# Optimization experiments

Measured on AMD Instinct MI355X. Metric: run time of the kernel, lower is better.

## Reference

```python
import jax, jax.numpy as jnp
import numpy as np

S, B, D, Z, C, H = 256, 1024, 64, 32, 64, 128
L = 2 * S + 3  # len(ext_ts); _xs[0::2][1:-1] must match xs -> L = 2*S+3


def setup_inputs() -> dict:
    key = jax.random.key(0)
    ks = jax.random.split(key, 16)

    def xavier(k, out_d, in_d):
        lim = float(np.sqrt(6.0 / (in_d + out_d)))
        return jax.random.uniform(k, (out_d, in_d), minval=-lim, maxval=lim, dtype=jnp.float32)

    bias = lambda n: jnp.full((n,), 0.01, jnp.float32)  # m.bias.data.fill_(0.01)

    return {
        "xs": jax.random.normal(ks[0], (S, B, D), jnp.float32),
        "ext_ts": jnp.arange(L, dtype=jnp.float32) * 0.01,  # spacing <= dt=0.02 -> 1 euler step/interval
        "eps_z0": jax.random.normal(ks[1], (B, Z), jnp.float32),
        "dW": jax.random.normal(ks[2], (L - 1, B, Z), jnp.float32),  # standard normal; scaled by sqrt(dt) inside
        "gru_Wih": xavier(ks[3], 3 * H, D),
        "gru_Whh": xavier(ks[4], 3 * H, H),
        "gru_bih": jnp.zeros((3 * H,), jnp.float32),
        "gru_bhh": jnp.zeros((3 * H,), jnp.float32),
        "enc_W": xavier(ks[5], C, H), "enc_b": bias(C),
        "qz0_W": xavier(ks[6], 2 * Z, C), "qz0_b": bias(2 * Z),
        "f_W1": xavier(ks[7], H, Z + 1), "f_b1": bias(H),
        "f_W2": xavier(ks[8], H, H), "f_b2": bias(H),
        "f_W3": xavier(ks[9], Z, H), "f_b3": bias(Z),
        "g_W1": xavier(ks[10], H, Z + 1), "g_b1": bias(H),
        "g_W2": xavier(ks[11], Z, H), "g_b2": bias(Z),
        "proj_W": xavier(ks[12], D, Z), "proj_b": bias(D),
        "pz0_mean": jnp.zeros((1, Z), jnp.float32),
        "pz0_logstd": jnp.zeros((1, Z), jnp.float32),
    }


def reference(xs, ext_ts, eps_z0, dW, gru_Wih, gru_Whh, gru_bih, gru_bhh,
              enc_W, enc_b, qz0_W, qz0_b,
              f_W1, f_b1, f_W2, f_b2, f_W3, f_b3,
              g_W1, g_b1, g_W2, g_b2,
              proj_W, proj_b, pz0_mean, pz0_logstd):
    nb = xs.shape[1]
    # ---- Encoder: GRU over time-reversed xs; only ctx[0] (after flip-back) is
    # used, which equals lin(final hidden of the reversed-sequence GRU).
    x_rev = xs[::-1]
    gi_all = jnp.einsum('sbd,hd->sbh', x_rev, gru_Wih) + gru_bih  # (S,B,3H)

    def gru_step(h, gi_t):
        gh = h @ gru_Whh.T + gru_bhh
        i_r, i_z, i_n = jnp.split(gi_t, 3, axis=-1)
        h_r, h_z, h_n = jnp.split(gh, 3, axis=-1)
        r = jax.nn.sigmoid(i_r + h_r)
        zg = jax.nn.sigmoid(i_z + h_z)
        n = jnp.tanh(i_n + r * h_n)
        return (1.0 - zg) * n + zg * h, None

    hT, _ = jax.lax.scan(gru_step, jnp.zeros((nb, gru_Whh.shape[1]), xs.dtype), gi_all)
    ctx0 = hT @ enc_W.T + enc_b

    # ---- q(z0) and reparameterized sample
    q = ctx0 @ qz0_W.T + qz0_b
    qz0_mean, qz0_logstd = jnp.split(q, 2, axis=1)
    z0 = qz0_mean + jnp.exp(qz0_logstd) * eps_z0

    # ---- Euler-Maruyama SDE integration (diagonal noise), one step per interval
    dts = ext_ts[1:] - ext_ts[:-1]

    def sde_step(z, inp):
        t, dt, dw = inp
        tcol = jnp.broadcast_to(t.reshape(1, 1), (z.shape[0], 1)).astype(z.dtype)
        tz = jnp.concatenate([tcol, z], axis=1)  # (B, Z+1)
        h1 = jax.nn.relu(tz @ f_W1.T + f_b1)
        h2 = jax.nn.relu(h1 @ f_W2.T + f_b2)
        drift = h2 @ f_W3.T + f_b3
        gh = jax.nn.relu(tz @ g_W1.T + g_b1)
        diff = gh @ g_W2.T + g_b2
        z_new = z + drift * dt + diff * (jnp.sqrt(dt) * dw)
        return z_new, z_new

    _, zs_rest = jax.lax.scan(sde_step, z0, (ext_ts[:-1], dts, dW))
    zs = jnp.concatenate([z0[None], zs_rest], axis=0)  # (L,B,Z)

    # ---- project to data space and compute losses
    xs_hat = jnp.einsum('lbz,dz->lbd', zs, proj_W) + proj_b
    recon_xs = xs_hat[0::2][1:-1]   # (S,B,D)
    interp_xs = xs_hat[1::2][1:-1]  # (S-1,B,D)
    recon_loss = jnp.mean((recon_xs - xs) ** 2)

    # KL( N(qm, e^qls) || N(pm, e^pls) ), summed over latent, averaged over batch
    kl = (pz0_logstd - qz0_logstd
          + (jnp.exp(2.0 * qz0_logstd) + (qz0_mean - pz0_mean) ** 2)
          / (2.0 * jnp.exp(2.0 * pz0_logstd)) - 0.5)
    logqp0 = jnp.mean(jnp.sum(kl, axis=1))
    return recon_loss, logqp0, interp_xs
```

## Files before the change

### kernel.cpp

```cpp
#include <hip/hip_runtime.h>

typedef _Float16 f16;
typedef _Float16 h2 __attribute__((ext_vector_type(2)));
typedef _Float16 h8 __attribute__((ext_vector_type(8)));
typedef _Float16 v8h __attribute__((ext_vector_type(8)));
typedef _Float16 v4h __attribute__((ext_vector_type(4)));
typedef float    f4 __attribute__((ext_vector_type(4)));
typedef float    v4f __attribute__((ext_vector_type(4)));
typedef float    f2 __attribute__((ext_vector_type(2)));

#define S_  256
#define B_  1024
#define D_  64
#define H_  128
#define Z_  32
#define BD_ (B_*D_)
#define NSTEP 514

#define BAR() do { \
  asm volatile("s_waitcnt lgkmcnt(0)" ::: "memory"); \
  __builtin_amdgcn_s_barrier(); \
} while (0)

__device__ __forceinline__ h8 ld8(const float* p) {
  f4 a = *(const f4*)p;
  f4 b = *(const f4*)(p + 4);
  h8 w;
  w[0]=(f16)a[0]; w[1]=(f16)a[1]; w[2]=(f16)a[2]; w[3]=(f16)a[3];
  w[4]=(f16)b[0]; w[5]=(f16)b[1]; w[6]=(f16)b[2]; w[7]=(f16)b[3];
  return w;
}

__device__ __forceinline__ float sigm(float x) { return 1.f / (1.f + __expf(-x)); }
__device__ __forceinline__ float tanh_(float x) {
  float e = __expf(-2.f * fabsf(x));
  float t = (1.f - e) / (1.f + e);
  return copysignf(t, x);
}

__global__ __launch_bounds__(256, 1) void gru_mfma_kernel(
    const float* __restrict__ xs, const float* __restrict__ Wih,
    const float* __restrict__ Whh, const float* __restrict__ bih,
    const float* __restrict__ bhh, float* __restrict__ hT)
{
  __shared__ f16 hB[2][16][136];

  const int t    = threadIdx.x;
  const int wid  = t >> 6;
  const int lane = t & 63;
  const int lr = lane & 15;
  const int lg = lane >> 4;
  const int r0 = blockIdx.x * 16;

  v8h whhR[2][4], whhZ[2][4], whhN[2][4];
  v8h wihR[2][2], wihZ[2][2], wihN[2][2];
  #pragma unroll
  for (int tt = 0; tt < 2; ++tt) {
    const int nr = wid*32 + tt*16 + lr;
    #pragma unroll
    for (int ks = 0; ks < 4; ++ks) {
      whhR[tt][ks] = ld8(Whh + (      nr)*H_ + ks*32 + lg*8);
      whhZ[tt][ks] = ld8(Whh + (128 + nr)*H_ + ks*32 + lg*8);
      whhN[tt][ks] = ld8(Whh + (256 + nr)*H_ + ks*32 + lg*8);
    }
    #pragma unroll
    for (int ks = 0; ks < 2; ++ks) {
      wihR[tt][ks] = ld8(Wih + (      nr)*D_ + ks*32 + lg*8);
      wihZ[tt][ks] = ld8(Wih + (128 + nr)*D_ + ks*32 + lg*8);
      wihN[tt][ks] = ld8(Wih + (256 + nr)*D_ + ks*32 + lg*8);
    }
  }
  v4f birh[2], bizh[2], binv[2], bhnv[2];
  #pragma unroll
  for (int tt = 0; tt < 2; ++tt) {
    const int nb = wid*32 + tt*16 + lg*4;
    v4f a = *(const v4f*)&bih[nb],     b = *(const v4f*)&bhh[nb];
    v4f c = *(const v4f*)&bih[128+nb], d = *(const v4f*)&bhh[128+nb];
    birh[tt] = a + b;
    bizh[tt] = c + d;
    binv[tt] = *(const v4f*)&bih[256+nb];
    bhnv[tt] = *(const v4f*)&bhh[256+nb];
  }

  for (int i = t; i < 16*136; i += 256) ((f16*)hB[0])[i] = (f16)0.f;
  v4f hm[2] = { {0.f,0.f,0.f,0.f}, {0.f,0.f,0.f,0.f} };
  const v4f zero4 = {0.f, 0.f, 0.f, 0.f};

  v8h bx0 = ld8(xs + (S_-1)*BD_ + (r0+lr)*D_ + lg*8);
  v8h bx1 = ld8(xs + (S_-1)*BD_ + (r0+lr)*D_ + 32 + lg*8);
  __syncthreads();

  int p = 0;
  #pragma unroll 1
  for (int s = 0; s < S_; ++s) {
    v8h nx0 = bx0, nx1 = bx1;
    if (s < S_-1) {
      const float* xp = xs + (S_-2-s)*BD_ + (r0+lr)*D_;
      nx0 = ld8(xp + lg*8);
      nx1 = ld8(xp + 32 + lg*8);
    }
    v8h bh[4];
    #pragma unroll
    for (int ks = 0; ks < 4; ++ks)
      bh[ks] = *(const v8h*)&hB[p][lr][ks*32 + lg*8];

    #pragma unroll
    for (int tt = 0; tt < 2; ++tt) {
      v4f ar  = __builtin_amdgcn_mfma_f32_16x16x32_f16(wihR[tt][0], bx0, zero4, 0,0,0);
      v4f az  = __builtin_amdgcn_mfma_f32_16x16x32_f16(wihZ[tt][0], bx0, zero4, 0,0,0);
      v4f anx = __builtin_amdgcn_mfma_f32_16x16x32_f16(wihN[tt][0], bx0, zero4, 0,0,0);
      ar  = __builtin_amdgcn_mfma_f32_16x16x32_f16(wihR[tt][1], bx1, ar,  0,0,0);
      az  = __builtin_amdgcn_mfma_f32_16x16x32_f16(wihZ[tt][1], bx1, az,  0,0,0);
      anx = __builtin_amdgcn_mfma_f32_16x16x32_f16(wihN[tt][1], bx1, anx, 0,0,0);
      v4f anh = zero4;
      #pragma unroll
      for (int ks = 0; ks < 4; ++ks) {
        ar  = __builtin_amdgcn_mfma_f32_16x16x32_f16(whhR[tt][ks], bh[ks], ar,  0,0,0);
        az  = __builtin_amdgcn_mfma_f32_16x16x32_f16(whhZ[tt][ks], bh[ks], az,  0,0,0);
        anh = __builtin_amdgcn_mfma_f32_16x16x32_f16(whhN[tt][ks], bh[ks], anh, 0,0,0);
      }
      v4h o;
      #pragma unroll
      for (int i = 0; i < 4; ++i) {
        float r  = sigm(ar[i] + birh[tt][i]);
        float zg = sigm(az[i] + bizh[tt][i]);
        float n  = tanh_(anx[i] + binv[tt][i] + r*(anh[i] + bhnv[tt][i]));
        hm[tt][i] = (1.f - zg)*n + zg*hm[tt][i];
        o[i] = (f16)hm[tt][i];
      }
      *(v4h*)&hB[p^1][lr][wid*32 + tt*16 + lg*4] = o;
    }
    BAR();
    p ^= 1;
    bx0 = nx0; bx1 = nx1;
  }

  #pragma unroll
  for (int tt = 0; tt < 2; ++tt)
    *(v4f*)&hT[(r0+lr)*H_ + wid*32 + tt*16 + lg*4] = hm[tt];
}

__global__ __launch_bounds__(256) void enc_kernel(
    const float* __restrict__ hT, const float* __restrict__ encW,
    const float* __restrict__ encB, const float* __restrict__ qW,
    const float* __restrict__ qB, const float* __restrict__ eps,
    const float* __restrict__ pm, const float* __restrict__ pls,
    float* __restrict__ z0, float* __restrict__ out)
{
  __shared__ float hTl[4][128];
  __shared__ float ctx[4][64];
  __shared__ float ql[4][64];
  const int t = threadIdx.x;
  const int b0 = blockIdx.x * 4;
  const int lb = t >> 6, j = t & 63;

  for (int i = t; i < 512; i += 256) hTl[i>>7][i&127] = hT[b0*H_ + i];
  __syncthreads();

  float acc = encB[j];
  #pragma unroll
  for (int k = 0; k < 128; k += 4) {
    f4 w = *(const f4*)&encW[j*128 + k];
    acc += hTl[lb][k]*w[0] + hTl[lb][k+1]*w[1] + hTl[lb][k+2]*w[2] + hTl[lb][k+3]*w[3];
  }
  ctx[lb][j] = acc;
  __syncthreads();

  float q = qB[j];
  #pragma unroll
  for (int k = 0; k < 64; k += 4) {
    f4 w = *(const f4*)&qW[j*64 + k];
    q += ctx[lb][k]*w[0] + ctx[lb][k+1]*w[1] + ctx[lb][k+2]*w[2] + ctx[lb][k+3]*w[3];
  }
  ql[lb][j] = q;
  __syncthreads();

  float kl = 0.f;
  if (j < 32) {
    float mean = ql[lb][j], ls = ql[lb][j+32];
    z0[(b0+lb)*Z_ + j] = mean + __expf(ls)*eps[(b0+lb)*Z_ + j];
    float pmj = pm[j], plsj = pls[j];
    float dm = mean - pmj;
    kl = plsj - ls + (__expf(2.f*ls) + dm*dm) / (2.f*__expf(2.f*plsj)) - 0.5f;
  }
  #pragma unroll
  for (int s2 = 32; s2 > 0; s2 >>= 1) kl += __shfl_down(kl, s2, 64);
  if (j == 0) atomicAdd(out + 1, kl * (1.f/1024.f));
}

__global__ __launch_bounds__(256, 1) void sde_mfma_kernel(
    const float* __restrict__ z0, const float* __restrict__ ts,
    const float* __restrict__ dW, const float* __restrict__ xs,
    const float* __restrict__ fW1, const float* __restrict__ fb1,
    const float* __restrict__ fW2, const float* __restrict__ fb2,
    const float* __restrict__ fW3, const float* __restrict__ fb3,
    const float* __restrict__ gW1, const float* __restrict__ gb1,
    const float* __restrict__ gW2, const float* __restrict__ gb2,
    const float* __restrict__ pW, const float* __restrict__ pb,
    float* __restrict__ out)
{
  __shared__ f16 Xa[16*72];
  __shared__ f16 h1A[16*168];
  __shared__ f16 ghA[16*168];
  __shared__ f16 h2A[16*168];
  __shared__ float tsL[516];
  __shared__ float lred[4];

  const int t    = threadIdx.x;
  const int wid  = t >> 6;
  const int lane = t & 63;
  const int lr = lane & 15;
  const int lg = lane >> 4;
  const int r0 = blockIdx.x * 16;
  const int wz = wid & 1;

  v8h w1r[8];
  #pragma unroll
  for (int nl = 0; nl < 4; ++nl) {
    const int n = wid*4 + nl;
    const float* src = (n < 8) ? (fW1 + (n*16+lr)*33) : (gW1 + ((n-8)*16+lr)*33);
    const float bsv  = (n < 8) ? fb1[n*16+lr] : gb1[(n-8)*16+lr];
    #pragma unroll
    for (int ks = 0; ks < 2; ++ks) {
      v8h w;
      #pragma unroll
      for (int j = 0; j < 8; ++j) {
        const int kp = ks*32 + lg*8 + j;
        float v;
        if (kp < 32)                   v = src[1+kp];
        else if (kp == 32 || kp == 34) v = src[0];
        else if (kp == 33)             v = bsv;
        else                           v = 0.f;
        w[j] = (f16)v;
      }
      w1r[nl*2+ks] = w;
    }
  }
  v8h w2r[10];
  #pragma unroll
  for (int nl = 0; nl < 2; ++nl) {
    const int n = wid*2 + nl;
    const float* src = fW2 + (n*16+lr)*128;
    const float bsv = fb2[n*16+lr];
    #pragma unroll
    for (int ks = 0; ks < 5; ++ks) {
      v8h w;
      #pragma unroll
      for (int j = 0; j < 8; ++j) {
        const int kp = ks*32 + lg*8 + j;
        float v = (kp < 128) ? src[kp] : ((kp == 128) ? bsv : 0.f);
        w[j] = (f16)v;
      }
      w2r[nl*5+ks] = w;
    }
  }
  v8h w3d[5], w3g[5];
  {
    const float* sd = fW3 + (wz*16+lr)*128;
    const float* sg = gW2 + (wz*16+lr)*128;
    const float bd = fb3[wz*16+lr], bg = gb2[wz*16+lr];
    #pragma unroll
    for (int ks = 0; ks < 5; ++ks) {
      v8h wd, wg;
      #pragma unroll
      for (int j = 0; j < 8; ++j) {
        const int kp = ks*32 + lg*8 + j;
        wd[j] = (f16)((kp < 128) ? sd[kp] : ((kp == 128) ? bd : 0.f));
        wg[j] = (f16)((kp < 128) ? sg[kp] : ((kp == 128) ? bg : 0.f));
      }
      w3d[ks] = wd; w3g[ks] = wg;
    }
  }
  v8h pwr[2];
  {
    const float* sp = pW + (wid*16+lr)*32;
    const float bp = pb[wid*16+lr];
    #pragma unroll
    for (int ks = 0; ks < 2; ++ks) {
      v8h w;
      #pragma unroll
      for (int j = 0; j < 8; ++j) {
        const int kp = ks*32 + lg*8 + j;
        w[j] = (f16)((kp < 32) ? sp[kp] : ((kp == 33) ? bp : 0.f));
      }
      pwr[ks] = w;
    }
  }

  for (int i = t; i < 16*72; i += 256) Xa[i] = (f16)0.f;
  for (int i = t; i < 16*168; i += 256) {
    h1A[i] = (f16)0.f; ghA[i] = (f16)0.f; h2A[i] = (f16)0.f;
  }
  for (int i = t; i < 515; i += 256) tsL[i] = ts[i];
  __syncthreads();
  if (t < 16) {
    Xa[t*72 + 33] = (f16)1.f;
    h1A[t*168 + 128] = (f16)1.f;
    ghA[t*168 + 128] = (f16)1.f;
    h2A[t*168 + 128] = (f16)1.f;
    const float t0 = tsL[0];
    const f16 th = (f16)t0;
    Xa[t*72 + 32] = th;
    Xa[t*72 + 34] = (f16)(t0 - (float)th);
  }
  const v4f zero4 = {0.f, 0.f, 0.f, 0.f};
  v4f zm = zero4;
  if (wid < 2) {
    zm = *(const v4f*)&z0[(r0+lr)*Z_ + wid*16 + lg*4];
    v4h a;
    #pragma unroll
    for (int i = 0; i < 4; ++i) a[i] = (f16)zm[i];
    *(v4h*)&Xa[lr*72 + wid*16 + lg*4] = a;
  }
  float loss = 0.f;
  __syncthreads();

  #pragma unroll 1
  for (int l = 0; l < NSTEP; ++l) {
    const float dt  = tsL[l+1] - tsL[l];
    const float sdt = sqrtf(dt);
    const int ln = l + 1;
    const bool ev = ((ln & 1) == 0) && ln >= 2 && ln <= 512;
    const bool od = ((ln & 1) == 1) && ln >= 3 && ln <= 511;

    v4f dwv = zero4;
    if (wid < 2) dwv = *(const v4f*)&dW[(l*B_ + r0 + lr)*Z_ + wid*16 + lg*4];
    v4f xv = zero4;
    if (ev) xv = *(const v4f*)&xs[(((ln-2)>>1)*B_ + r0 + lr)*D_ + wid*16 + lg*4];

    {
      const v8h bx0 = *(const v8h*)&Xa[lr*72 +  0 + lg*8];
      const v8h bx1 = *(const v8h*)&Xa[lr*72 + 32 + lg*8];
      #pragma unroll
      for (int nl = 0; nl < 4; ++nl) {
        v4f acc = __builtin_amdgcn_mfma_f32_16x16x32_f16(w1r[nl*2+0], bx0, zero4, 0, 0, 0);
        acc = __builtin_amdgcn_mfma_f32_16x16x32_f16(w1r[nl*2+1], bx1, acc, 0, 0, 0);
        v4h o;
        #pragma unroll
        for (int i = 0; i < 4; ++i) o[i] = (f16)fmaxf(acc[i], 0.f);
        if (wid < 2) *(v4h*)&h1A[lr*168 + (wid*4+nl)*16 + lg*4] = o;
        else         *(v4h*)&ghA[lr*168 + ((wid-2)*4+nl)*16 + lg*4] = o;
      }
    }
    BAR();

    {
      v8h bh[5];
      #pragma unroll
      for (int ks = 0; ks < 5; ++ks) bh[ks] = *(const v8h*)&h1A[lr*168 + ks*32 + lg*8];
      #pragma unroll
      for (int nl = 0; nl < 2; ++nl) {
        v4f acc = zero4;
        #pragma unroll
        for (int ks = 0; ks < 5; ++ks)
          acc = __builtin_amdgcn_mfma_f32_16x16x32_f16(w2r[nl*5+ks], bh[ks], acc, 0, 0, 0);
        v4h o;
        #pragma unroll
        for (int i = 0; i < 4; ++i) o[i] = (f16)fmaxf(acc[i], 0.f);
        *(v4h*)&h2A[lr*168 + (wid*2+nl)*16 + lg*4] = o;
      }
    }
    BAR();

    if (wid < 2) {
      v4f dac = zero4, fac = zero4;
      #pragma unroll
      for (int ks = 0; ks < 5; ++ks) {
        const v8h b2f = *(const v8h*)&h2A[lr*168 + ks*32 + lg*8];
        const v8h bgf = *(const v8h*)&ghA[lr*168 + ks*32 + lg*8];
        dac = __builtin_amdgcn_mfma_f32_16x16x32_f16(w3d[ks], b2f, dac, 0, 0, 0);
        fac = __builtin_amdgcn_mfma_f32_16x16x32_f16(w3g[ks], bgf, fac, 0, 0, 0);
      }
      #pragma unroll
      for (int i = 0; i < 4; ++i) zm[i] += dac[i]*dt + fac[i]*(sdt*dwv[i]);
      v4h a;
      #pragma unroll
      for (int i = 0; i < 4; ++i) a[i] = (f16)zm[i];
      *(v4h*)&Xa[lr*72 + wid*16 + lg*4] = a;
    } else if (wid == 3 && lg == 0) {
      const float tn = tsL[l+1];
      const f16 th = (f16)tn;
      Xa[lr*72 + 32] = th;
      Xa[lr*72 + 34] = (f16)(tn - (float)th);
    }
    BAR();

    if (ev || od) {
      const v8h px0 = *(const v8h*)&Xa[lr*72 +  0 + lg*8];
      const v8h px1 = *(const v8h*)&Xa[lr*72 + 32 + lg*8];
      v4f a = __builtin_amdgcn_mfma_f32_16x16x32_f16(pwr[0], px0, zero4, 0, 0, 0);
      v4f p = __builtin_amdgcn_mfma_f32_16x16x32_f16(pwr[1], px1, a, 0, 0, 0);
      if (ev) {
        #pragma unroll
        for (int i = 0; i < 4; ++i) { float d = p[i] - xv[i]; loss = fmaf(d, d, loss); }
      } else {
        float* op = out + 2 + (((ln-3)>>1)*B_ + r0 + lr)*D_ + wid*16 + lg*4;
        *(f2*)&op[0] = (f2){p[0], p[1]};
        *(f2*)&op[2] = (f2){p[2], p[3]};
      }
    }
  }

  #pragma unroll
  for (int s2 = 32; s2 > 0; s2 >>= 1) loss += __shfl_down(loss, s2, 64);
  if (lane == 0) lred[wid] = loss;
  __syncthreads();
  if (t == 0)
    atomicAdd(out + 0, (lred[0] + lred[1] + lred[2] + lred[3]) * (1.f/16777216.f));
}

extern "C" void kernel_launch(void* const* d_in, const int* in_sizes, int n_in,
                              void* d_out, int out_size, void* d_ws, size_t ws_size,
                              hipStream_t stream) {
  (void)in_sizes; (void)n_in; (void)out_size; (void)ws_size;
  const float* xs   = (const float*)d_in[0];
  const float* ts   = (const float*)d_in[1];
  const float* eps  = (const float*)d_in[2];
  const float* dWp  = (const float*)d_in[3];
  const float* Wih  = (const float*)d_in[4];
  const float* Whh  = (const float*)d_in[5];
  const float* bih  = (const float*)d_in[6];
  const float* bhh  = (const float*)d_in[7];
  const float* encW = (const float*)d_in[8];
  const float* encB = (const float*)d_in[9];
  const float* qW   = (const float*)d_in[10];
  const float* qB   = (const float*)d_in[11];
  const float* fW1  = (const float*)d_in[12];
  const float* fb1  = (const float*)d_in[13];
  const float* fW2  = (const float*)d_in[14];
  const float* fb2  = (const float*)d_in[15];
  const float* fW3  = (const float*)d_in[16];
  const float* fb3  = (const float*)d_in[17];
  const float* gW1  = (const float*)d_in[18];
  const float* gb1  = (const float*)d_in[19];
  const float* gW2  = (const float*)d_in[20];
  const float* gb2  = (const float*)d_in[21];
  const float* pW   = (const float*)d_in[22];
  const float* pb   = (const float*)d_in[23];
  const float* pm   = (const float*)d_in[24];
  const float* pls  = (const float*)d_in[25];

  float* out = (float*)d_out;
  float* ws  = (float*)d_ws;
  float* hT = ws;
  float* z0 = ws + 131072;

  hipMemsetAsync(d_out, 0, 2*sizeof(float), stream);
  hipLaunchKernelGGL(gru_mfma_kernel, dim3(64), dim3(256), 0, stream,
                     xs, Wih, Whh, bih, bhh, hT);
  hipLaunchKernelGGL(enc_kernel, dim3(256), dim3(256), 0, stream,
                     hT, encW, encB, qW, qB, eps, pm, pls, z0, out);
  hipLaunchKernelGGL(sde_mfma_kernel, dim3(64), dim3(256), 0, stream,
                     z0, ts, dWp, xs, fW1, fb1, fW2, fb2, fW3, fb3,
                     gW1, gb1, gW2, gb2, pW, pb, out);
}
```

Before: 1.274 ms.

## Defer SDE projection to next step and split MFMA accumulator chains

In the SDE loop, the output projection and its loss/store no longer run in a separate phase after the last barrier. It is computed at the start of the next iteration from the same latent buffer, and its epilogue sits in the second phase, which removes a serial tail from each step. The W2, W3 and GRU MFMA reductions are split into independent accumulator chains that are summed at the end, to shorten dependent MFMA latency. The GRU also issues its raw fp32 x loads early and defers the f16 conversion until after the barrier. This adds register pressure and carries extra state across iterations.

New measurement: 1.064 ms. 16.5% less time.

```diff
diff --git a/kernel.cpp b/kernel.cpp
--- a/kernel.cpp
+++ b/kernel.cpp
@@ -22,13 +22,17 @@
   __builtin_amdgcn_s_barrier(); \
 } while (0)
 
-__device__ __forceinline__ h8 ld8(const float* p) {
-  f4 a = *(const f4*)p;
-  f4 b = *(const f4*)(p + 4);
+__device__ __forceinline__ h8 cvt8(f4 a, f4 b) {
   h8 w;
   w[0]=(f16)a[0]; w[1]=(f16)a[1]; w[2]=(f16)a[2]; w[3]=(f16)a[3];
   w[4]=(f16)b[0]; w[5]=(f16)b[1]; w[6]=(f16)b[2]; w[7]=(f16)b[3];
   return w;
+}
+
+__device__ __forceinline__ h8 ld8(const float* p) {
+  f4 a = *(const f4*)p;
+  f4 b = *(const f4*)(p + 4);
+  return cvt8(a, b);
 }
 
 __device__ __forceinline__ float sigm(float x) { return 1.f / (1.f + __expf(-x)); }
@@ -93,11 +97,14 @@
   int p = 0;
   #pragma unroll 1
   for (int s = 0; s < S_; ++s) {
-    v8h nx0 = bx0, nx1 = bx1;
-    if (s < S_-1) {
+    f4 ra0 = zero4, rb0 = zero4, ra1 = zero4, rb1 = zero4;
+    const bool have = (s < S_-1);
+    if (have) {
       const float* xp = xs + (S_-2-s)*BD_ + (r0+lr)*D_;
-      nx0 = ld8(xp + lg*8);
-      nx1 = ld8(xp + 32 + lg*8);
+      ra0 = *(const f4*)(xp + lg*8);
+      rb0 = *(const f4*)(xp + lg*8 + 4);
+      ra1 = *(const f4*)(xp + 32 + lg*8);
+      rb1 = *(const f4*)(xp + 32 + lg*8 + 4);
     }
     v8h bh[4];
     #pragma unroll
@@ -106,24 +113,24 @@
 
     #pragma unroll
     for (int tt = 0; tt < 2; ++tt) {
-      v4f ar  = __builtin_amdgcn_mfma_f32_16x16x32_f16(wihR[tt][0], bx0, zero4, 0,0,0);
-      v4f az  = __builtin_amdgcn_mfma_f32_16x16x32_f16(wihZ[tt][0], bx0, zero4, 0,0,0);
+      v4f ri  = __builtin_amdgcn_mfma_f32_16x16x32_f16(wihR[tt][0], bx0, zero4, 0,0,0);
+      v4f zi  = __builtin_amdgcn_mfma_f32_16x16x32_f16(wihZ[tt][0], bx0, zero4, 0,0,0);
       v4f anx = __builtin_amdgcn_mfma_f32_16x16x32_f16(wihN[tt][0], bx0, zero4, 0,0,0);
-      ar  = __builtin_amdgcn_mfma_f32_16x16x32_f16(wihR[tt][1], bx1, ar,  0,0,0);
-      az  = __builtin_amdgcn_mfma_f32_16x16x32_f16(wihZ[tt][1], bx1, az,  0,0,0);
+      ri  = __builtin_amdgcn_mfma_f32_16x16x32_f16(wihR[tt][1], bx1, ri,  0,0,0);
+      zi  = __builtin_amdgcn_mfma_f32_16x16x32_f16(wihZ[tt][1], bx1, zi,  0,0,0);
       anx = __builtin_amdgcn_mfma_f32_16x16x32_f16(wihN[tt][1], bx1, anx, 0,0,0);
-      v4f anh = zero4;
+      v4f rh = zero4, zh = zero4, anh = zero4;
       #pragma unroll
       for (int ks = 0; ks < 4; ++ks) {
-        ar  = __builtin_amdgcn_mfma_f32_16x16x32_f16(whhR[tt][ks], bh[ks], ar,  0,0,0);
-        az  = __builtin_amdgcn_mfma_f32_16x16x32_f16(whhZ[tt][ks], bh[ks], az,  0,0,0);
+        rh  = __builtin_amdgcn_mfma_f32_16x16x32_f16(whhR[tt][ks], bh[ks], rh,  0,0,0);
+        zh  = __builtin_amdgcn_mfma_f32_16x16x32_f16(whhZ[tt][ks], bh[ks], zh,  0,0,0);
         anh = __builtin_amdgcn_mfma_f32_16x16x32_f16(whhN[tt][ks], bh[ks], anh, 0,0,0);
       }
       v4h o;
       #pragma unroll
       for (int i = 0; i < 4; ++i) {
-        float r  = sigm(ar[i] + birh[tt][i]);
-        float zg = sigm(az[i] + bizh[tt][i]);
+        float r  = sigm(ri[i] + rh[i] + birh[tt][i]);
+        float zg = sigm(zi[i] + zh[i] + bizh[tt][i]);
         float n  = tanh_(anx[i] + binv[tt][i] + r*(anh[i] + bhnv[tt][i]));
         hm[tt][i] = (1.f - zg)*n + zg*hm[tt][i];
         o[i] = (f16)hm[tt][i];
@@ -131,8 +138,8 @@
       *(v4h*)&hB[p^1][lr][wid*32 + tt*16 + lg*4] = o;
     }
     BAR();
+    if (have) { bx0 = cvt8(ra0, rb0); bx1 = cvt8(ra1, rb1); }
     p ^= 1;
-    bx0 = nx0; bx1 = nx1;
   }
 
   #pragma unroll
@@ -313,6 +320,9 @@
     *(v4h*)&Xa[lr*72 + wid*16 + lg*4] = a;
   }
   float loss = 0.f;
+  bool pev = false, pod = false;
+  int  pln = 0;
+  v4f  pxv = zero4;
   __syncthreads();
 
   #pragma unroll 1
@@ -325,9 +335,10 @@
 
     v4f dwv = zero4;
     if (wid < 2) dwv = *(const v4f*)&dW[(l*B_ + r0 + lr)*Z_ + wid*16 + lg*4];
-    v4f xv = zero4;
-    if (ev) xv = *(const v4f*)&xs[(((ln-2)>>1)*B_ + r0 + lr)*D_ + wid*16 + lg*4];
-
+    v4f xvl = zero4;
+    if (ev) xvl = *(const v4f*)&xs[(((ln-2)>>1)*B_ + r0 + lr)*D_ + wid*16 + lg*4];
+
+    v4f pj = zero4;
     {
       const v8h bx0 = *(const v8h*)&Xa[lr*72 +  0 + lg*8];
       const v8h bx1 = *(const v8h*)&Xa[lr*72 + 32 + lg*8];
@@ -341,6 +352,10 @@
         if (wid < 2) *(v4h*)&h1A[lr*168 + (wid*4+nl)*16 + lg*4] = o;
         else         *(v4h*)&ghA[lr*168 + ((wid-2)*4+nl)*16 + lg*4] = o;
       }
+      if (pev || pod) {
+        pj = __builtin_amdgcn_mfma_f32_16x16x32_f16(pwr[0], bx0, zero4, 0, 0, 0);
+        pj = __builtin_amdgcn_mfma_f32_16x16x32_f16(pwr[1], bx1, pj, 0, 0, 0);
+      }
     }
     BAR();
 
@@ -348,12 +363,26 @@
       v8h bh[5];
       #pragma unroll
       for (int ks = 0; ks < 5; ++ks) bh[ks] = *(const v8h*)&h1A[lr*168 + ks*32 + lg*8];
+      v4f a0[2], a1[2];
       #pragma unroll
       for (int nl = 0; nl < 2; ++nl) {
-        v4f acc = zero4;
+        a0[nl] = __builtin_amdgcn_mfma_f32_16x16x32_f16(w2r[nl*5+0], bh[0], zero4, 0, 0, 0);
+        a1[nl] = __builtin_amdgcn_mfma_f32_16x16x32_f16(w2r[nl*5+1], bh[1], zero4, 0, 0, 0);
+        a0[nl] = __builtin_amdgcn_mfma_f32_16x16x32_f16(w2r[nl*5+2], bh[2], a0[nl], 0, 0, 0);
+        a1[nl] = __builtin_amdgcn_mfma_f32_16x16x32_f16(w2r[nl*5+3], bh[3], a1[nl], 0, 0, 0);
+        a0[nl] = __builtin_amdgcn_mfma_f32_16x16x32_f16(w2r[nl*5+4], bh[4], a0[nl], 0, 0, 0);
+      }
+      if (pev) {
         #pragma unroll
-        for (int ks = 0; ks < 5; ++ks)
-          acc = __builtin_amdgcn_mfma_f32_16x16x32_f16(w2r[nl*5+ks], bh[ks], acc, 0, 0, 0);
+        for (int i = 0; i < 4; ++i) { float d = pj[i] - pxv[i]; loss = fmaf(d, d, loss); }
+      } else if (pod) {
+        float* op = out + 2 + (((pln-3)>>1)*B_ + r0 + lr)*D_ + wid*16 + lg*4;
+        *(f2*)&op[0] = (f2){pj[0], pj[1]};
+        *(f2*)&op[2] = (f2){pj[2], pj[3]};
+      }
+      #pragma unroll
+      for (int nl = 0; nl < 2; ++nl) {
+        v4f acc = a0[nl] + a1[nl];
         v4h o;
         #pragma unroll
         for (int i = 0; i < 4; ++i) o[i] = (f16)fmaxf(acc[i], 0.f);
@@ -363,16 +392,26 @@
     BAR();
 
     if (wid < 2) {
-      v4f dac = zero4, fac = zero4;
+      v4f d0 = zero4, d1 = zero4, f0 = zero4, f1 = zero4;
+      v8h b2f[5], bgf[5];
       #pragma unroll
       for (int ks = 0; ks < 5; ++ks) {
-        const v8h b2f = *(const v8h*)&h2A[lr*168 + ks*32 + lg*8];
-        const v8h bgf = *(const v8h*)&ghA[lr*168 + ks*32 + lg*8];
-        dac = __builtin_amdgcn_mfma_f32_16x16x32_f16(w3d[ks], b2f, dac, 0, 0, 0);
-        fac = __builtin_amdgcn_mfma_f32_16x16x32_f16(w3g[ks], bgf, fac, 0, 0, 0);
-      }
-      #pragma unroll
-      for (int i = 0; i < 4; ++i) zm[i] += dac[i]*dt + fac[i]*(sdt*dwv[i]);
+        b2f[ks] = *(const v8h*)&h2A[lr*168 + ks*32 + lg*8];
+        bgf[ks] = *(const v8h*)&ghA[lr*168 + ks*32 + lg*8];
+      }
+      d0 = __builtin_amdgcn_mfma_f32_16x16x32_f16(w3d[0], b2f[0], d0, 0, 0, 0);
+      f0 = __builtin_amdgcn_mfma_f32_16x16x32_f16(w3g[0], bgf[0], f0, 0, 0, 0);
+      d1 = __builtin_amdgcn_mfma_f32_16x16x32_f16(w3d[1], b2f[1], d1, 0, 0, 0);
+      f1 = __builtin_amdgcn_mfma_f32_16x16x32_f16(w3g[1], bgf[1], f1, 0, 0, 0);
+      d0 = __builtin_amdgcn_mfma_f32_16x16x32_f16(w3d[2], b2f[2], d0, 0, 0, 0);
+      f0 = __builtin_amdgcn_mfma_f32_16x16x32_f16(w3g[2], bgf[2], f0, 0, 0, 0);
+      d1 = __builtin_amdgcn_mfma_f32_16x16x32_f16(w3d[3], b2f[3], d1, 0, 0, 0);
+      f1 = __builtin_amdgcn_mfma_f32_16x16x32_f16(w3g[3], bgf[3], f1, 0, 0, 0);
+      d0 = __builtin_amdgcn_mfma_f32_16x16x32_f16(w3d[4], b2f[4], d0, 0, 0, 0);
+      f0 = __builtin_amdgcn_mfma_f32_16x16x32_f16(w3g[4], bgf[4], f0, 0, 0, 0);
+      #pragma unroll
+      for (int i = 0; i < 4; ++i)
+        zm[i] += (d0[i] + d1[i])*dt + (f0[i] + f1[i])*(sdt*dwv[i]);
       v4h a;
       #pragma unroll
       for (int i = 0; i < 4; ++i) a[i] = (f16)zm[i];
@@ -385,20 +424,8 @@
     }
     BAR();
 
-    if (ev || od) {
-      const v8h px0 = *(const v8h*)&Xa[lr*72 +  0 + lg*8];
-      const v8h px1 = *(const v8h*)&Xa[lr*72 + 32 + lg*8];
-      v4f a = __builtin_amdgcn_mfma_f32_16x16x32_f16(pwr[0], px0, zero4, 0, 0, 0);
-      v4f p = __builtin_amdgcn_mfma_f32_16x16x32_f16(pwr[1], px1, a, 0, 0, 0);
-      if (ev) {
-        #pragma unroll
-        for (int i = 0; i < 4; ++i) { float d = p[i] - xv[i]; loss = fmaf(d, d, loss); }
-      } else {
-        float* op = out + 2 + (((ln-3)>>1)*B_ + r0 + lr)*D_ + wid*16 + lg*4;
-        *(f2*)&op[0] = (f2){p[0], p[1]};
-        *(f2*)&op[2] = (f2){p[2], p[3]};
-      }
-    }
+    pev = ev; pod = od; pln = ln;
+    if (ev) pxv = xvl;
   }
 
   #pragma unroll
```
